# Kernel tuning notes

Measured on AMD Instinct MI355X. Metric: run time of the kernel, lower is better.

## Reference

```python
import jax, jax.numpy as jnp
import numpy as np

C1, C2 = 32, 16  # first_no_layer, second_no_layer
BN_EPS = 1e-5


def _irr(x, W, b):
    # Faithful port of irregular_convolution.forward.
    # x: [B, S, C, N, K] (torch layout with an extra seq axis).
    # torch: permute(0,1,3,2) then reshape([B, N, C*K]) -- a logical row-major
    # reshape of the transposed tensor (identical semantics in jnp).
    B, S, C, N, K = x.shape
    t = jnp.swapaxes(x, -1, -2).reshape(B, S, N, C * K)
    y = jnp.einsum('bsnm,om->bsno', t, W) + b  # tiny GEMM
    # permute(0,2,1).unsqueeze(-1) -> [B, S, O, N, 1]
    return jnp.moveaxis(y, -1, 2)[..., None]


def _prepare(y, neigh):
    # Faithful port of prepare_data: broadcast node row then masked_select.
    # y: [B, S, C, 1, N]; masked_select with a row-sorted kernel mask is a gather
    # of each node's sorted semantic neighbors: out[...,n,k] = y[...,0,neigh[n,k]].
    v = y[..., 0, :]          # [B, S, C, N]
    return v[..., neigh]      # [B, S, C, N, K]


def setup_inputs() -> dict:
    key = jax.random.key(0)
    ks = jax.random.split(key, 10)
    B, S, N, K = 8, 24, 4096, 9
    inp = {
        'input': jax.random.normal(ks[0], (B, S, N, K), dtype=jnp.float32),
        'neigh': jnp.sort(jax.random.randint(ks[1], (N, K), 0, N), axis=-1).astype(jnp.int32),
        'W1': jax.random.normal(ks[2], (C1, 1 * K), dtype=jnp.float32) * 0.05,
        'b1': jax.random.normal(ks[3], (C1,), dtype=jnp.float32) * 0.05,
        'W2': jax.random.normal(ks[4], (C2, C1 * K), dtype=jnp.float32) * 0.05,
        'b2': jax.random.normal(ks[5], (C2,), dtype=jnp.float32) * 0.05,
        'gamma': jnp.ones((C2,), dtype=jnp.float32),
        'beta': jnp.zeros((C2,), dtype=jnp.float32),
        'W3': jax.random.normal(ks[6], (1, C2 * K), dtype=jnp.float32) * 0.05,
        'b3': jax.random.normal(ks[7], (1,), dtype=jnp.float32) * 0.05,
    }
    return inp


def reference(input, neigh, W1, b1, W2, b2, gamma, beta, W3, b3):
    x = input[:, :, None]                                   # [B,S,1,N,K]
    h = jax.nn.relu(_irr(x, W1, b1))                        # [B,S,32,N,1]
    h = jnp.swapaxes(h, -1, -2)                             # [B,S,32,1,N]
    g = _prepare(h, neigh)                                  # [B,S,32,N,K]
    y = _irr(g, W2, b2)                                     # [B,S,16,N,1]
    # BatchNorm2d (training mode): stats over batch+spatial, per seq step & channel
    mean = jnp.mean(y, axis=(0, 3, 4), keepdims=True)
    var = jnp.var(y, axis=(0, 3, 4), keepdims=True)
    gb = (1, 1, C2, 1, 1)
    y = gamma.reshape(gb) * (y - mean) * jax.lax.rsqrt(var + BN_EPS) + beta.reshape(gb)
    y = jax.nn.relu(y)
    y = jnp.swapaxes(y, -1, -2)                             # [B,S,16,1,N]
    g = _prepare(y, neigh)                                  # [B,S,16,N,K]
    y = jax.nn.relu(_irr(g, W3, b3))                        # [B,S,1,N,1]
    return jnp.squeeze(y, axis=(2, 4))                      # [B,S,N]
```

## Files before the change

kernel.cpp:

```cpp
#include <hip/hip_runtime.h>
#include <hip/hip_bf16.h>

#define NB 8
#define NS 24
#define NN 4096
#define NC1 32
#define NC2 16
#define BN_COUNT 32768.0f

typedef float f32x4 __attribute__((ext_vector_type(4)));
typedef short bf16x8 __attribute__((ext_vector_type(8)));
union U8 { int4 i; bf16x8 b; };

#define PERM_LO 0x05040100u
#define PERM_HI 0x07060302u


__global__ void k_tables(const int* __restrict__ neigh,
                         int* __restrict__ G2M, int* __restrict__ G3Q,
                         const float* __restrict__ W2,
                         __hip_bfloat16* __restrict__ W2B) {
    int j = blockIdx.x * 256 + threadIdx.x;
    if (j < 36864) {
        int j8 = j & 7;
        int tkbl = j >> 3;
        int l = tkbl & 63;
        int tkb = tkbl >> 6;
        int t = tkb / 9, kb = tkb - t * 9;
        int r = t * 16 + (l & 15);
        int k = kb * 32 + ((l >> 4) << 3) + j8;
        int rem = r * 288 + k;
        G2M[j] = neigh[(rem & 4095) * 9 + (rem >> 12)];
    } else if (j < 73728) {
        int tt = j - 36864;
        int e = tt >> 2, jj = tt & 3;
        int m4 = e >> 8, r = e & 255;
        int m = m4 * 4 + jj;
        int rem = r * 144 + m;
        G3Q[tt] = neigh[(rem & 4095) * 9 + (rem >> 12)];
    } else {
        int jj = j - 73728;
        int kb = jj >> 9;
        int rest = jj & 511;
        int l = rest >> 3, j8 = rest & 7;
        int o = l & 15;
        int k = kb * 32 + ((l >> 4) << 3) + j8;
        W2B[jj] = __float2bfloat16(W2[o * 288 + k]);
    }
}

__global__ __launch_bounds__(256) void k_layer1(const float* __restrict__ input,
                                                const float* __restrict__ W1,
                                                const float* __restrict__ b1,
                                                __hip_bfloat16* __restrict__ h) {
    __shared__ __align__(16) float win[4680];
    __shared__ __align__(16) float corner[72];
    int blk = blockIdx.x;
    int w = blk & 7, bs = blk >> 3;
    int n0 = w * 512;
    const float* A = input + (size_t)bs * 36864;
    int base = n0 * 9;
    int cnt4 = min(4680, 36864 - base) >> 2;
    const float4* A4 = (const float4*)(A + base);
    float4* win4 = (float4*)win;
    for (int j = threadIdx.x; j < cnt4; j += 256) win4[j] = A4[j];
    if (threadIdx.x < 18) ((float4*)corner)[threadIdx.x] = ((const float4*)A)[threadIdx.x];
    __syncthreads();

    __hip_bfloat16* hb = h + (size_t)bs * (NC1 * NN);
    for (int i = threadIdx.x; i < 522; i += 256) {
        int j = i / 58, off = i - j * 58;
        int x = j * 4096 + n0;
        int pstart = (x + 8) / 9;
        int pend   = (x + 520) / 9;
        int p = pstart + off;
        if (p >= pend) continue;
        int nf = (p * 9) & 4095;
        float v[9];
        int wb = (nf - n0) * 9 + j;
        if (nf <= 4087) {
#pragma unroll
            for (int m = 0; m < 9; m++) v[m] = win[wb + 9 * m];
        } else {
            int nw = 4096 - nf;
#pragma unroll
            for (int m = 0; m < 9; m++)
                v[m] = (m < nw) ? win[wb + 9 * m]
                                : corner[(nf + m - 4096) * 9 + j + 1];
        }
#pragma unroll 4
        for (int c = 0; c < 32; c++) {
            float acc = b1[c];
#pragma unroll
            for (int m = 0; m < 9; m++) acc = fmaf(v[m], W1[c * 9 + m], acc);
            hb[c * NN + p] = __float2bfloat16(fmaxf(acc, 0.f));
        }
    }
}

__global__ __launch_bounds__(256) void k_layer2(const __hip_bfloat16* __restrict__ h,
                                                const int4* __restrict__ G2M4,
                                                const int4* __restrict__ W2B4,
                                                const float* __restrict__ b2,
                                                __hip_bfloat16* __restrict__ y2,
                                                float* __restrict__ psum,
                                                float* __restrict__ psq) {
    __shared__ __align__(16) unsigned int hl[4096];
    __shared__ float4 wsum[4][16];
    int blk = blockIdx.x;
    int cp = blk & 15, bs = blk >> 4;
    int c0 = cp * 2;
    const unsigned int* hb0 = (const unsigned int*)(h + ((size_t)bs * NC1 + c0) * NN);
    const unsigned int* hb1 = (const unsigned int*)(h + ((size_t)bs * NC1 + c0 + 1) * NN);
    uint2* hl2 = (uint2*)hl;
    for (int j = threadIdx.x; j < 2048; j += 256) {
        unsigned int u0 = hb0[j], u1 = hb1[j];
        uint2 p;
        p.x = __builtin_amdgcn_perm(u1, u0, PERM_LO);
        p.y = __builtin_amdgcn_perm(u1, u0, PERM_HI);
        hl2[j] = p;
    }
    __syncthreads();

    int tid = threadIdx.x;
    int l = tid & 63, w = tid >> 6;
    int o = l & 15, q = l >> 4;

    U8 bfrag[9];
#pragma unroll
    for (int kb = 0; kb < 9; kb++) bfrag[kb].i = W2B4[kb * 64 + l];
    float bb = b2[o];

    float s1c0 = 0.f, s2c0 = 0.f, s1c1 = 0.f, s2c1 = 0.f;

    for (int tt = 0; tt < 2; tt++) {
        int t = w * 2 + tt;
        f32x4 ac0 = {0.f, 0.f, 0.f, 0.f};
        f32x4 ac1 = {0.f, 0.f, 0.f, 0.f};
        const int4* gp = G2M4 + (size_t)(t * 9) * 128 + l * 2;
#pragma unroll
        for (int kb = 0; kb < 9; kb++) {
            int4 ia = gp[kb * 128];
            int4 ib = gp[kb * 128 + 1];
            unsigned int d0 = hl[ia.x], d1 = hl[ia.y], d2 = hl[ia.z], d3 = hl[ia.w];
            unsigned int d4 = hl[ib.x], d5 = hl[ib.y], d6 = hl[ib.z], d7 = hl[ib.w];
            U8 a0, a1;
            a0.i.x = __builtin_amdgcn_perm(d1, d0, PERM_LO);
            a0.i.y = __builtin_amdgcn_perm(d3, d2, PERM_LO);
            a0.i.z = __builtin_amdgcn_perm(d5, d4, PERM_LO);
            a0.i.w = __builtin_amdgcn_perm(d7, d6, PERM_LO);
            a1.i.x = __builtin_amdgcn_perm(d1, d0, PERM_HI);
            a1.i.y = __builtin_amdgcn_perm(d3, d2, PERM_HI);
            a1.i.z = __builtin_amdgcn_perm(d5, d4, PERM_HI);
            a1.i.w = __builtin_amdgcn_perm(d7, d6, PERM_HI);
            ac0 = __builtin_amdgcn_mfma_f32_16x16x32_bf16(a0.b, bfrag[kb].b, ac0, 0, 0, 0);
            ac1 = __builtin_amdgcn_mfma_f32_16x16x32_bf16(a1.b, bfrag[kb].b, ac1, 0, 0, 0);
        }
        __hip_bfloat16* yb = y2 + (size_t)bs * (NC2 * NN) + o * NN;
        int rbase = t * 16 + q * 4;
#pragma unroll
        for (int i = 0; i < 4; i++) {
            float v0 = ac0[i] + bb;
            float v1 = ac1[i] + bb;
            int n0 = c0 * 128 + rbase + i;
            yb[n0]       = __float2bfloat16(v0);
            yb[n0 + 128] = __float2bfloat16(v1);
            s1c0 += v0; s2c0 += v0 * v0;
            s1c1 += v1; s2c1 += v1 * v1;
        }
    }

    s1c0 += __shfl_xor(s1c0, 16); s1c0 += __shfl_xor(s1c0, 32);
    s2c0 += __shfl_xor(s2c0, 16); s2c0 += __shfl_xor(s2c0, 32);
    s1c1 += __shfl_xor(s1c1, 16); s1c1 += __shfl_xor(s1c1, 32);
    s2c1 += __shfl_xor(s2c1, 16); s2c1 += __shfl_xor(s2c1, 32);
    if (l < 16) wsum[w][l] = make_float4(s1c0, s2c0, s1c1, s2c1);
    __syncthreads();
    if (tid < 32) {
        int ch = tid >> 4, oo = tid & 15;
        float a = 0.f, b = 0.f;
#pragma unroll
        for (int ww = 0; ww < 4; ww++) {
            float4 v = wsum[ww][oo];
            a += ch ? v.z : v.x;
            b += ch ? v.w : v.y;
        }
        int s_idx = bs % NS, b_idx = bs / NS;
        int srow = s_idx * 16 + oo;
        int col  = b_idx * 32 + (c0 + ch);
        psum[srow * 256 + col] = a;
        psq [srow * 256 + col] = b;
    }
}

__global__ __launch_bounds__(256) void k_bnstat(const float* __restrict__ psum,
                                                const float* __restrict__ psq,
                                                const float* __restrict__ gamma,
                                                const float* __restrict__ beta,
                                                float* __restrict__ scale,
                                                float* __restrict__ shift) {
    __shared__ float l1[4], l2[4];
    int row = blockIdx.x;
    int t = threadIdx.x;
    float s = psum[row * 256 + t], q = psq[row * 256 + t];
    for (int off = 32; off; off >>= 1) {
        s += __shfl_down(s, off);
        q += __shfl_down(q, off);
    }
    if ((t & 63) == 0) { l1[t >> 6] = s; l2[t >> 6] = q; }
    __syncthreads();
    if (t == 0) {
        s = l1[0] + l1[1] + l1[2] + l1[3];
        q = l2[0] + l2[1] + l2[2] + l2[3];
        float mean = s * (1.0f / BN_COUNT);
        float var  = q * (1.0f / BN_COUNT) - mean * mean;
        float inv  = rsqrtf(var + 1e-5f);
        int o = row & 15;
        float sc = gamma[o] * inv;
        scale[row] = sc;
        shift[row] = beta[o] - mean * sc;
    }
}

__global__ __launch_bounds__(256) void k_layer3(const __hip_bfloat16* __restrict__ y2,
                                                const int* __restrict__ G3Q,
                                                const float* __restrict__ scale,
                                                const float* __restrict__ shift,
                                                const float* __restrict__ W3,
                                                const float* __restrict__ b3,
                                                float* __restrict__ out) {
    __shared__ __align__(16) unsigned int zl[4096];
    int blk = blockIdx.x;
    int cpp = blk & 7, bs = blk >> 3;
    int c0 = cpp * 2;
    int s = bs % NS;
    float sc0 = scale[s * 16 + c0],     sh0 = shift[s * 16 + c0];
    float sc1 = scale[s * 16 + c0 + 1], sh1 = shift[s * 16 + c0 + 1];
    const unsigned int* yb0 = (const unsigned int*)(y2 + ((size_t)bs * NC2 + c0) * NN);
    const unsigned int* yb1 = (const unsigned int*)(y2 + ((size_t)bs * NC2 + c0 + 1) * NN);
    uint2* zl2 = (uint2*)zl;
    for (int j = threadIdx.x; j < 2048; j += 256) {
        unsigned int u0 = yb0[j], u1 = yb1[j];
        float a0 = fmaxf(fmaf(__uint_as_float(u0 << 16),          sc0, sh0), 0.f);
        float a1 = fmaxf(fmaf(__uint_as_float(u0 & 0xffff0000u),  sc0, sh0), 0.f);
        float b0 = fmaxf(fmaf(__uint_as_float(u1 << 16),          sc1, sh1), 0.f);
        float b1 = fmaxf(fmaf(__uint_as_float(u1 & 0xffff0000u),  sc1, sh1), 0.f);
        __hip_bfloat16 ba0 = __float2bfloat16(a0), bb0 = __float2bfloat16(b0);
        __hip_bfloat16 ba1 = __float2bfloat16(a1), bb1 = __float2bfloat16(b1);
        uint2 p;
        p.x = (unsigned int)*(unsigned short*)&ba0 | ((unsigned int)*(unsigned short*)&bb0 << 16);
        p.y = (unsigned int)*(unsigned short*)&ba1 | ((unsigned int)*(unsigned short*)&bb1 << 16);
        zl2[j] = p;
    }
    __syncthreads();
    int r = threadIdx.x;
    const int4* gq = (const int4*)G3Q;
    float acc0 = b3[0], acc1 = b3[0];
    for (int m4 = 0; m4 < 36; m4 += 2) {
        int4 qa = gq[m4 * 256 + r];
        int4 qb = gq[(m4 + 1) * 256 + r];
        unsigned int dd[8] = {zl[qa.x], zl[qa.y], zl[qa.z], zl[qa.w],
                              zl[qb.x], zl[qb.y], zl[qb.z], zl[qb.w]};
#pragma unroll
        for (int jj = 0; jj < 8; jj++) {
            float wv = W3[m4 * 4 + jj];
            acc0 = fmaf(__uint_as_float(dd[jj] << 16),         wv, acc0);
            acc1 = fmaf(__uint_as_float(dd[jj] & 0xffff0000u), wv, acc1);
        }
    }
    float* ob = out + (size_t)bs * NN + c0 * 256 + r;
    ob[0]   = fmaxf(acc0, 0.f);
    ob[256] = fmaxf(acc1, 0.f);
}

extern "C" void kernel_launch(void* const* d_in, const int* in_sizes, int n_in,
                              void* d_out, int out_size, void* d_ws, size_t ws_size,
                              hipStream_t stream) {
    const float* input = (const float*)d_in[0];
    const int*   neigh = (const int*)d_in[1];
    const float* W1    = (const float*)d_in[2];
    const float* b1    = (const float*)d_in[3];
    const float* W2    = (const float*)d_in[4];
    const float* b2    = (const float*)d_in[5];
    const float* gamma = (const float*)d_in[6];
    const float* beta  = (const float*)d_in[7];
    const float* W3    = (const float*)d_in[8];
    const float* b3    = (const float*)d_in[9];
    float* out = (float*)d_out;

    char* ws = (char*)d_ws;
    int*            G2M   = (int*)            (ws);
    int*            G3Q   = (int*)            (ws + 147456);
    __hip_bfloat16* W2B   = (__hip_bfloat16*) (ws + 294912);
    __hip_bfloat16* h     = (__hip_bfloat16*) (ws + 304128);
    __hip_bfloat16* y2    = (__hip_bfloat16*) (ws + 50635776);
    float*          psum  = (float*)          (ws + 75801600);
    float*          psq   = (float*)          (ws + 76194816);
    float*          scale = (float*)          (ws + 76588032);
    float*          shift = (float*)          (ws + 76589568);

    k_tables<<<306, 256, 0, stream>>>(neigh, G2M, G3Q, W2, W2B);
    k_layer1<<<1536, 256, 0, stream>>>(input, W1, b1, h);
    k_layer2<<<3072, 256, 0, stream>>>(h, (const int4*)G2M, (const int4*)W2B,
                                       b2, y2, psum, psq);
    k_bnstat<<<384, 256, 0, stream>>>(psum, psq, gamma, beta, scale, shift);
    k_layer3<<<1536, 256, 0, stream>>>(y2, G3Q, scale, shift, W3, b3, out);
}
```

Before: 161.8 us.

## Pack channels in groups of eight and use MFMA for layer three

Intermediate activations h and y2 are stored channel-interleaved, eight bf16 channels per node in one uint4. Each gathered LDS read in layers 2 and 3 now serves eight channels instead of two, which cuts gather and index-table traffic per MFMA. Layer 3 is rewritten as a zero-padded 16x16x32 bf16 MFMA product in place of scalar FMAs. This wastes 15 of 16 output columns and most of the padded K dimension, and the BN partial-sum layout is narrowed to 64 columns to match.

Measured after the change: 161.6 us. No clear change (-0.2%).

```diff
diff --git a/kernel.cpp b/kernel.cpp
--- a/kernel.cpp
+++ b/kernel.cpp
@@ -11,15 +11,21 @@
 typedef float f32x4 __attribute__((ext_vector_type(4)));
 typedef short bf16x8 __attribute__((ext_vector_type(8)));
 union U8 { int4 i; bf16x8 b; };
+union Q  { uint4 v; unsigned u[4]; };
 
 #define PERM_LO 0x05040100u
 #define PERM_HI 0x07060302u
 
+__device__ __forceinline__ unsigned short bfbits(float x) {
+    __hip_bfloat16 h = __float2bfloat16(x);
+    return *(unsigned short*)&h;
+}
 
 __global__ void k_tables(const int* __restrict__ neigh,
-                         int* __restrict__ G2M, int* __restrict__ G3Q,
-                         const float* __restrict__ W2,
-                         __hip_bfloat16* __restrict__ W2B) {
+                         int* __restrict__ G2M, int* __restrict__ G3M,
+                         const float* __restrict__ W2, const float* __restrict__ W3,
+                         __hip_bfloat16* __restrict__ W2B,
+                         __hip_bfloat16* __restrict__ W3B) {
     int j = blockIdx.x * 256 + threadIdx.x;
     if (j < 36864) {
         int j8 = j & 7;
@@ -31,28 +37,40 @@
         int k = kb * 32 + ((l >> 4) << 3) + j8;
         int rem = r * 288 + k;
         G2M[j] = neigh[(rem & 4095) * 9 + (rem >> 12)];
-    } else if (j < 73728) {
-        int tt = j - 36864;
-        int e = tt >> 2, jj = tt & 3;
-        int m4 = e >> 8, r = e & 255;
-        int m = m4 * 4 + jj;
-        int rem = r * 144 + m;
-        G3Q[tt] = neigh[(rem & 4095) * 9 + (rem >> 12)];
-    } else {
-        int jj = j - 73728;
+    } else if (j < 77824) {
+        int t2 = j - 36864;
+        int j8 = t2 & 7;
+        int tkbl = t2 >> 3;
+        int l = tkbl & 63;
+        int tkb = tkbl >> 6;
+        int t = tkb / 5, kb = tkb - t * 5;
+        int r = t * 16 + (l & 15);
+        int k = kb * 32 + ((l >> 4) << 3) + j8;
+        int rem = r * 144 + k;
+        G3M[t2] = (k < 144) ? neigh[(rem & 4095) * 9 + (rem >> 12)] : 0;
+    } else if (j < 82432) {
+        int jj = j - 77824;
         int kb = jj >> 9;
         int rest = jj & 511;
         int l = rest >> 3, j8 = rest & 7;
         int o = l & 15;
         int k = kb * 32 + ((l >> 4) << 3) + j8;
         W2B[jj] = __float2bfloat16(W2[o * 288 + k]);
+    } else {
+        int jj = j - 82432;
+        int kb = jj >> 9;
+        int rest = jj & 511;
+        int l = rest >> 3, j8 = rest & 7;
+        int o = l & 15;
+        int k = kb * 32 + ((l >> 4) << 3) + j8;
+        W3B[jj] = __float2bfloat16((o == 0 && k < 144) ? W3[k] : 0.f);
     }
 }
 
 __global__ __launch_bounds__(256) void k_layer1(const float* __restrict__ input,
                                                 const float* __restrict__ W1,
                                                 const float* __restrict__ b1,
-                                                __hip_bfloat16* __restrict__ h) {
+                                                uint4* __restrict__ hp) {
     __shared__ __align__(16) float win[4680];
     __shared__ __align__(16) float corner[72];
     int blk = blockIdx.x;
@@ -67,7 +85,6 @@
     if (threadIdx.x < 18) ((float4*)corner)[threadIdx.x] = ((const float4*)A)[threadIdx.x];
     __syncthreads();
 
-    __hip_bfloat16* hb = h + (size_t)bs * (NC1 * NN);
     for (int i = threadIdx.x; i < 522; i += 256) {
         int j = i / 58, off = i - j * 58;
         int x = j * 4096 + n0;
@@ -88,130 +105,118 @@
                 v[m] = (m < nw) ? win[wb + 9 * m]
                                 : corner[(nf + m - 4096) * 9 + j + 1];
         }
+        float acc[32];
 #pragma unroll 4
         for (int c = 0; c < 32; c++) {
-            float acc = b1[c];
-#pragma unroll
-            for (int m = 0; m < 9; m++) acc = fmaf(v[m], W1[c * 9 + m], acc);
-            hb[c * NN + p] = __float2bfloat16(fmaxf(acc, 0.f));
-        }
-    }
-}
-
-__global__ __launch_bounds__(256) void k_layer2(const __hip_bfloat16* __restrict__ h,
+            float a = b1[c];
+#pragma unroll
+            for (int m = 0; m < 9; m++) a = fmaf(v[m], W1[c * 9 + m], a);
+            acc[c] = fmaxf(a, 0.f);
+        }
+#pragma unroll
+        for (int pl = 0; pl < 4; pl++) {
+            uint4 d;
+            d.x = (unsigned)bfbits(acc[pl * 8 + 0]) | ((unsigned)bfbits(acc[pl * 8 + 1]) << 16);
+            d.y = (unsigned)bfbits(acc[pl * 8 + 2]) | ((unsigned)bfbits(acc[pl * 8 + 3]) << 16);
+            d.z = (unsigned)bfbits(acc[pl * 8 + 4]) | ((unsigned)bfbits(acc[pl * 8 + 5]) << 16);
+            d.w = (unsigned)bfbits(acc[pl * 8 + 6]) | ((unsigned)bfbits(acc[pl * 8 + 7]) << 16);
+            hp[((size_t)pl * 192 + bs) * NN + p] = d;
+        }
+    }
+}
+
+__global__ __launch_bounds__(256) void k_layer2(const uint4* __restrict__ hp,
                                                 const int4* __restrict__ G2M4,
                                                 const int4* __restrict__ W2B4,
                                                 const float* __restrict__ b2,
-                                                __hip_bfloat16* __restrict__ y2,
+                                                __hip_bfloat16* __restrict__ y2p,
                                                 float* __restrict__ psum,
                                                 float* __restrict__ psq) {
-    __shared__ __align__(16) unsigned int hl[4096];
-    __shared__ float4 wsum[4][16];
+    __shared__ __align__(16) uint4 hl[4096];
+    __shared__ float wred[2][4][16];
     int blk = blockIdx.x;
-    int cp = blk & 15, bs = blk >> 4;
-    int c0 = cp * 2;
-    const unsigned int* hb0 = (const unsigned int*)(h + ((size_t)bs * NC1 + c0) * NN);
-    const unsigned int* hb1 = (const unsigned int*)(h + ((size_t)bs * NC1 + c0 + 1) * NN);
-    uint2* hl2 = (uint2*)hl;
-    for (int j = threadIdx.x; j < 2048; j += 256) {
-        unsigned int u0 = hb0[j], u1 = hb1[j];
-        uint2 p;
-        p.x = __builtin_amdgcn_perm(u1, u0, PERM_LO);
-        p.y = __builtin_amdgcn_perm(u1, u0, PERM_HI);
-        hl2[j] = p;
-    }
+    int rh = blk & 1, pl = (blk >> 1) & 3, bs = blk >> 3;
+    const uint4* hb = hp + ((size_t)pl * 192 + bs) * NN;
+    for (int j = threadIdx.x; j < 4096; j += 256) hl[j] = hb[j];
     __syncthreads();
 
     int tid = threadIdx.x;
     int l = tid & 63, w = tid >> 6;
     int o = l & 15, q = l >> 4;
+    int t = rh * 4 + w;
 
     U8 bfrag[9];
 #pragma unroll
     for (int kb = 0; kb < 9; kb++) bfrag[kb].i = W2B4[kb * 64 + l];
     float bb = b2[o];
 
-    float s1c0 = 0.f, s2c0 = 0.f, s1c1 = 0.f, s2c1 = 0.f;
-
-    for (int tt = 0; tt < 2; tt++) {
-        int t = w * 2 + tt;
-        f32x4 ac0 = {0.f, 0.f, 0.f, 0.f};
-        f32x4 ac1 = {0.f, 0.f, 0.f, 0.f};
-        const int4* gp = G2M4 + (size_t)(t * 9) * 128 + l * 2;
-#pragma unroll
-        for (int kb = 0; kb < 9; kb++) {
-            int4 ia = gp[kb * 128];
-            int4 ib = gp[kb * 128 + 1];
-            unsigned int d0 = hl[ia.x], d1 = hl[ia.y], d2 = hl[ia.z], d3 = hl[ia.w];
-            unsigned int d4 = hl[ib.x], d5 = hl[ib.y], d6 = hl[ib.z], d7 = hl[ib.w];
-            U8 a0, a1;
-            a0.i.x = __builtin_amdgcn_perm(d1, d0, PERM_LO);
-            a0.i.y = __builtin_amdgcn_perm(d3, d2, PERM_LO);
-            a0.i.z = __builtin_amdgcn_perm(d5, d4, PERM_LO);
-            a0.i.w = __builtin_amdgcn_perm(d7, d6, PERM_LO);
-            a1.i.x = __builtin_amdgcn_perm(d1, d0, PERM_HI);
-            a1.i.y = __builtin_amdgcn_perm(d3, d2, PERM_HI);
-            a1.i.z = __builtin_amdgcn_perm(d5, d4, PERM_HI);
-            a1.i.w = __builtin_amdgcn_perm(d7, d6, PERM_HI);
-            ac0 = __builtin_amdgcn_mfma_f32_16x16x32_bf16(a0.b, bfrag[kb].b, ac0, 0, 0, 0);
-            ac1 = __builtin_amdgcn_mfma_f32_16x16x32_bf16(a1.b, bfrag[kb].b, ac1, 0, 0, 0);
-        }
-        __hip_bfloat16* yb = y2 + (size_t)bs * (NC2 * NN) + o * NN;
-        int rbase = t * 16 + q * 4;
+    f32x4 acc[8];
+#pragma unroll
+    for (int c = 0; c < 8; c++) acc[c] = (f32x4){0.f, 0.f, 0.f, 0.f};
+
+    const int4* gp = G2M4 + (size_t)(t * 9) * 128 + l * 2;
+#pragma unroll
+    for (int kb = 0; kb < 9; kb++) {
+        int4 ia = gp[kb * 128];
+        int4 ib = gp[kb * 128 + 1];
+        Q d[8];
+        d[0].v = hl[ia.x]; d[1].v = hl[ia.y]; d[2].v = hl[ia.z]; d[3].v = hl[ia.w];
+        d[4].v = hl[ib.x]; d[5].v = hl[ib.y]; d[6].v = hl[ib.z]; d[7].v = hl[ib.w];
+#pragma unroll
+        for (int c = 0; c < 8; c++) {
+            const int q2 = c >> 1;
+            const unsigned sel = (c & 1) ? PERM_HI : PERM_LO;
+            U8 Af;
+            Af.i.x = __builtin_amdgcn_perm(d[1].u[q2], d[0].u[q2], sel);
+            Af.i.y = __builtin_amdgcn_perm(d[3].u[q2], d[2].u[q2], sel);
+            Af.i.z = __builtin_amdgcn_perm(d[5].u[q2], d[4].u[q2], sel);
+            Af.i.w = __builtin_amdgcn_perm(d[7].u[q2], d[6].u[q2], sel);
+            acc[c] = __builtin_amdgcn_mfma_f32_16x16x32_bf16(Af.b, bfrag[kb].b, acc[c], 0, 0, 0);
+        }
+    }
+
+    float s1 = 0.f, s2 = 0.f;
+    int rbase = t * 16 + q * 4;
+    __hip_bfloat16* ypl = y2p + (((size_t)(o >> 3) * 192 + bs) * NN) * 8 + (o & 7);
+#pragma unroll
+    for (int c = 0; c < 8; c++) {
+        int C = pl * 8 + c;
 #pragma unroll
         for (int i = 0; i < 4; i++) {
-            float v0 = ac0[i] + bb;
-            float v1 = ac1[i] + bb;
-            int n0 = c0 * 128 + rbase + i;
-            yb[n0]       = __float2bfloat16(v0);
-            yb[n0 + 128] = __float2bfloat16(v1);
-            s1c0 += v0; s2c0 += v0 * v0;
-            s1c1 += v1; s2c1 += v1 * v1;
-        }
-    }
-
-    s1c0 += __shfl_xor(s1c0, 16); s1c0 += __shfl_xor(s1c0, 32);
-    s2c0 += __shfl_xor(s2c0, 16); s2c0 += __shfl_xor(s2c0, 32);
-    s1c1 += __shfl_xor(s1c1, 16); s1c1 += __shfl_xor(s1c1, 32);
-    s2c1 += __shfl_xor(s2c1, 16); s2c1 += __shfl_xor(s2c1, 32);
-    if (l < 16) wsum[w][l] = make_float4(s1c0, s2c0, s1c1, s2c1);
+            float v = acc[c][i] + bb;
+            s1 += v; s2 += v * v;
+            int n = C * 128 + rbase + i;
+            ypl[(size_t)n * 8] = __float2bfloat16(v);
+        }
+    }
+    s1 += __shfl_xor(s1, 16); s1 += __shfl_xor(s1, 32);
+    s2 += __shfl_xor(s2, 16); s2 += __shfl_xor(s2, 32);
+    if (l < 16) { wred[0][w][l] = s1; wred[1][w][l] = s2; }
     __syncthreads();
-    if (tid < 32) {
-        int ch = tid >> 4, oo = tid & 15;
-        float a = 0.f, b = 0.f;
-#pragma unroll
-        for (int ww = 0; ww < 4; ww++) {
-            float4 v = wsum[ww][oo];
-            a += ch ? v.z : v.x;
-            b += ch ? v.w : v.y;
-        }
-        int s_idx = bs % NS, b_idx = bs / NS;
-        int srow = s_idx * 16 + oo;
-        int col  = b_idx * 32 + (c0 + ch);
-        psum[srow * 256 + col] = a;
-        psq [srow * 256 + col] = b;
-    }
-}
-
-__global__ __launch_bounds__(256) void k_bnstat(const float* __restrict__ psum,
-                                                const float* __restrict__ psq,
-                                                const float* __restrict__ gamma,
-                                                const float* __restrict__ beta,
-                                                float* __restrict__ scale,
-                                                float* __restrict__ shift) {
-    __shared__ float l1[4], l2[4];
+    if (tid < 16) {
+        float a = wred[0][0][tid] + wred[0][1][tid] + wred[0][2][tid] + wred[0][3][tid];
+        float b = wred[1][0][tid] + wred[1][1][tid] + wred[1][2][tid] + wred[1][3][tid];
+        int srow = (bs % NS) * 16 + tid;
+        int col  = (bs / NS) * 8 + pl * 2 + rh;
+        psum[srow * 64 + col] = a;
+        psq [srow * 64 + col] = b;
+    }
+}
+
+__global__ __launch_bounds__(64) void k_bnstat(const float* __restrict__ psum,
+                                               const float* __restrict__ psq,
+                                               const float* __restrict__ gamma,
+                                               const float* __restrict__ beta,
+                                               float* __restrict__ scale,
+                                               float* __restrict__ shift) {
     int row = blockIdx.x;
     int t = threadIdx.x;
-    float s = psum[row * 256 + t], q = psq[row * 256 + t];
+    float s = psum[row * 64 + t], q = psq[row * 64 + t];
     for (int off = 32; off; off >>= 1) {
         s += __shfl_down(s, off);
         q += __shfl_down(q, off);
     }
-    if ((t & 63) == 0) { l1[t >> 6] = s; l2[t >> 6] = q; }
-    __syncthreads();
     if (t == 0) {
-        s = l1[0] + l1[1] + l1[2] + l1[3];
-        q = l2[0] + l2[1] + l2[2] + l2[3];
         float mean = s * (1.0f / BN_COUNT);
         float var  = q * (1.0f / BN_COUNT) - mean * mean;
         float inv  = rsqrtf(var + 1e-5f);
@@ -222,55 +227,86 @@
     }
 }
 
-__global__ __launch_bounds__(256) void k_layer3(const __hip_bfloat16* __restrict__ y2,
-                                                const int* __restrict__ G3Q,
+__global__ __launch_bounds__(256) void k_layer3(const uint4* __restrict__ y2p,
+                                                const int4* __restrict__ G3M4,
+                                                const int4* __restrict__ W3B4,
                                                 const float* __restrict__ scale,
                                                 const float* __restrict__ shift,
-                                                const float* __restrict__ W3,
                                                 const float* __restrict__ b3,
                                                 float* __restrict__ out) {
-    __shared__ __align__(16) unsigned int zl[4096];
+    __shared__ __align__(16) uint4 zl[4096];
     int blk = blockIdx.x;
-    int cpp = blk & 7, bs = blk >> 3;
-    int c0 = cpp * 2;
+    int rh = blk & 1, pl = (blk >> 1) & 1, bs = blk >> 2;
     int s = bs % NS;
-    float sc0 = scale[s * 16 + c0],     sh0 = shift[s * 16 + c0];
-    float sc1 = scale[s * 16 + c0 + 1], sh1 = shift[s * 16 + c0 + 1];
-    const unsigned int* yb0 = (const unsigned int*)(y2 + ((size_t)bs * NC2 + c0) * NN);
-    const unsigned int* yb1 = (const unsigned int*)(y2 + ((size_t)bs * NC2 + c0 + 1) * NN);
-    uint2* zl2 = (uint2*)zl;
-    for (int j = threadIdx.x; j < 2048; j += 256) {
-        unsigned int u0 = yb0[j], u1 = yb1[j];
-        float a0 = fmaxf(fmaf(__uint_as_float(u0 << 16),          sc0, sh0), 0.f);
-        float a1 = fmaxf(fmaf(__uint_as_float(u0 & 0xffff0000u),  sc0, sh0), 0.f);
-        float b0 = fmaxf(fmaf(__uint_as_float(u1 << 16),          sc1, sh1), 0.f);
-        float b1 = fmaxf(fmaf(__uint_as_float(u1 & 0xffff0000u),  sc1, sh1), 0.f);
-        __hip_bfloat16 ba0 = __float2bfloat16(a0), bb0 = __float2bfloat16(b0);
-        __hip_bfloat16 ba1 = __float2bfloat16(a1), bb1 = __float2bfloat16(b1);
-        uint2 p;
-        p.x = (unsigned int)*(unsigned short*)&ba0 | ((unsigned int)*(unsigned short*)&bb0 << 16);
-        p.y = (unsigned int)*(unsigned short*)&ba1 | ((unsigned int)*(unsigned short*)&bb1 << 16);
-        zl2[j] = p;
+    float sc[8], sh[8];
+#pragma unroll
+    for (int jj = 0; jj < 8; jj++) {
+        sc[jj] = scale[s * 16 + pl * 8 + jj];
+        sh[jj] = shift[s * 16 + pl * 8 + jj];
+    }
+    const uint4* yb = y2p + ((size_t)pl * 192 + bs) * NN;
+    for (int j = threadIdx.x; j < 4096; j += 256) {
+        uint4 u = yb[j];
+        unsigned r[4] = {u.x, u.y, u.z, u.w};
+        uint4 pk;
+        unsigned* pp = (unsigned*)&pk;
+#pragma unroll
+        for (int dd = 0; dd < 4; dd++) {
+            float lo = fmaxf(fmaf(__uint_as_float(r[dd] << 16),         sc[dd*2],   sh[dd*2]),   0.f);
+            float hi = fmaxf(fmaf(__uint_as_float(r[dd] & 0xffff0000u), sc[dd*2+1], sh[dd*2+1]), 0.f);
+            unsigned ulo = __float_as_uint(lo) + 0x8000u;
+            unsigned uhi = __float_as_uint(hi) + 0x8000u;
+            pp[dd] = __builtin_amdgcn_perm(uhi, ulo, PERM_HI);
+        }
+        zl[j] = pk;
     }
     __syncthreads();
-    int r = threadIdx.x;
-    const int4* gq = (const int4*)G3Q;
-    float acc0 = b3[0], acc1 = b3[0];
-    for (int m4 = 0; m4 < 36; m4 += 2) {
-        int4 qa = gq[m4 * 256 + r];
-        int4 qb = gq[(m4 + 1) * 256 + r];
-        unsigned int dd[8] = {zl[qa.x], zl[qa.y], zl[qa.z], zl[qa.w],
-                              zl[qb.x], zl[qb.y], zl[qb.z], zl[qb.w]};
-#pragma unroll
-        for (int jj = 0; jj < 8; jj++) {
-            float wv = W3[m4 * 4 + jj];
-            acc0 = fmaf(__uint_as_float(dd[jj] << 16),         wv, acc0);
-            acc1 = fmaf(__uint_as_float(dd[jj] & 0xffff0000u), wv, acc1);
-        }
-    }
-    float* ob = out + (size_t)bs * NN + c0 * 256 + r;
-    ob[0]   = fmaxf(acc0, 0.f);
-    ob[256] = fmaxf(acc1, 0.f);
+
+    int tid = threadIdx.x;
+    int l = tid & 63, w = tid >> 6;
+    int o = l & 15, q = l >> 4;
+    float b3v = b3[0];
+
+    U8 bfrag[5];
+#pragma unroll
+    for (int kb = 0; kb < 5; kb++) bfrag[kb].i = W3B4[kb * 64 + l];
+
+#pragma unroll
+    for (int tt = 0; tt < 2; tt++) {
+        int t = rh * 8 + w * 2 + tt;
+        f32x4 acc[8];
+#pragma unroll
+        for (int c = 0; c < 8; c++) acc[c] = (f32x4){0.f, 0.f, 0.f, 0.f};
+        const int4* gp = G3M4 + (size_t)(t * 5) * 128 + l * 2;
+#pragma unroll
+        for (int kb = 0; kb < 5; kb++) {
+            int4 ia = gp[kb * 128];
+            int4 ib = gp[kb * 128 + 1];
+            Q d[8];
+            d[0].v = zl[ia.x]; d[1].v = zl[ia.y]; d[2].v = zl[ia.z]; d[3].v = zl[ia.w];
+            d[4].v = zl[ib.x]; d[5].v = zl[ib.y]; d[6].v = zl[ib.z]; d[7].v = zl[ib.w];
+#pragma unroll
+            for (int c = 0; c < 8; c++) {
+                const int q2 = c >> 1;
+                const unsigned sel = (c & 1) ? PERM_HI : PERM_LO;
+                U8 Af;
+                Af.i.x = __builtin_amdgcn_perm(d[1].u[q2], d[0].u[q2], sel);
+                Af.i.y = __builtin_amdgcn_perm(d[3].u[q2], d[2].u[q2], sel);
+                Af.i.z = __builtin_amdgcn_perm(d[5].u[q2], d[4].u[q2], sel);
+                Af.i.w = __builtin_amdgcn_perm(d[7].u[q2], d[6].u[q2], sel);
+                acc[c] = __builtin_amdgcn_mfma_f32_16x16x32_bf16(Af.b, bfrag[kb].b, acc[c], 0, 0, 0);
+            }
+        }
+        if (o == 0) {
+            int rbase = t * 16 + q * 4;
+            float* ob = out + (size_t)bs * NN + pl * 8 * 256 + rbase;
+#pragma unroll
+            for (int c = 0; c < 8; c++)
+#pragma unroll
+                for (int i = 0; i < 4; i++)
+                    ob[c * 256 + i] = fmaxf(acc[c][i] + b3v, 0.f);
+        }
+    }
 }
 
 extern "C" void kernel_launch(void* const* d_in, const int* in_sizes, int n_in,
@@ -290,19 +326,21 @@
 
     char* ws = (char*)d_ws;
     int*            G2M   = (int*)            (ws);
-    int*            G3Q   = (int*)            (ws + 147456);
-    __hip_bfloat16* W2B   = (__hip_bfloat16*) (ws + 294912);
-    __hip_bfloat16* h     = (__hip_bfloat16*) (ws + 304128);
-    __hip_bfloat16* y2    = (__hip_bfloat16*) (ws + 50635776);
-    float*          psum  = (float*)          (ws + 75801600);
-    float*          psq   = (float*)          (ws + 76194816);
-    float*          scale = (float*)          (ws + 76588032);
-    float*          shift = (float*)          (ws + 76589568);
-
-    k_tables<<<306, 256, 0, stream>>>(neigh, G2M, G3Q, W2, W2B);
+    int*            G3M   = (int*)            (ws + 147456);
+    __hip_bfloat16* W2B   = (__hip_bfloat16*) (ws + 311296);
+    __hip_bfloat16* W3B   = (__hip_bfloat16*) (ws + 320512);
+    uint4*          h     = (uint4*)          (ws + 325632);
+    __hip_bfloat16* y2    = (__hip_bfloat16*) (ws + 50657280);
+    float*          psum  = (float*)          (ws + 75823104);
+    float*          psq   = (float*)          (ws + 75921408);
+    float*          scale = (float*)          (ws + 76019712);
+    float*          shift = (float*)          (ws + 76021248);
+
+    k_tables<<<332, 256, 0, stream>>>(neigh, G2M, G3M, W2, W3, W2B, W3B);
     k_layer1<<<1536, 256, 0, stream>>>(input, W1, b1, h);
-    k_layer2<<<3072, 256, 0, stream>>>(h, (const int4*)G2M, (const int4*)W2B,
+    k_layer2<<<1536, 256, 0, stream>>>(h, (const int4*)G2M, (const int4*)W2B,
                                        b2, y2, psum, psq);
-    k_bnstat<<<384, 256, 0, stream>>>(psum, psq, gamma, beta, scale, shift);
-    k_layer3<<<1536, 256, 0, stream>>>(y2, G3Q, scale, shift, W3, b3, out);
-}
+    k_bnstat<<<384, 64, 0, stream>>>(psum, psq, gamma, beta, scale, shift);
+    k_layer3<<<768, 256, 0, stream>>>((const uint4*)y2, (const int4*)G3M,
+                                      (const int4*)W3B, scale, shift, b3, out);
+}
```
